# Kernel optimization log

Hardware: AMD Instinct MI355X
Metric: run time of the kernel (lower is better)

The kernel has to match this reference:

```python
import jax, jax.numpy as jnp
import numpy as np

B, L, D, H, S, V, K = 2, 64, 1024, 512, 50000, 40000, 32
SLM_LOGITS_SCALE = 0.1
BN_EPS = 1e-5


def setup_inputs() -> dict:
    key = jax.random.key(0)
    ks = jax.random.split(key, 8)
    return {
        "cached_embeddings": jax.random.normal(ks[0], (B, L, D), dtype=jnp.float32),
        "bn_gamma": jnp.ones((L,), jnp.float32),
        "bn_beta": jnp.zeros((L,), jnp.float32),
        "W1": jax.random.normal(ks[1], (D, H), dtype=jnp.float32) * 0.02,
        "b1": jnp.zeros((H,), jnp.float32),
        "W2": jax.random.normal(ks[2], (H, S), dtype=jnp.float32) * 0.02,
        "b2": jnp.zeros((S,), jnp.float32),
        "W_slm": jax.random.normal(ks[3], (H, V), dtype=jnp.float32) * 0.02,
        "b_slm": jnp.zeros((V,), jnp.float32),
        # fixed degree k=32 with values 1/min(deg,k) = 1/32 (full-degree rows)
        "sl_weights": jnp.full((S, K), 1.0 / K, jnp.float32),
        "sl_idx": jax.random.randint(ks[4], (S, K), 0, V, dtype=jnp.int32),
    }


def reference(cached_embeddings, bn_gamma, bn_beta, W1, b1, W2, b2,
              W_slm, b_slm, sl_weights, sl_idx):
    x = cached_embeddings  # [B, L, D]
    # BatchNorm1d(win_size): channels are sequence positions; stats over (B, D)
    mean = jnp.mean(x, axis=(0, 2), keepdims=True)
    var = jnp.var(x, axis=(0, 2), keepdims=True)
    xn = (x - mean) * jax.lax.rsqrt(var + BN_EPS)
    x = xn * bn_gamma[None, :, None] + bn_beta[None, :, None]
    # DenseEncoder: hidden + sense logits
    h = jax.nn.relu(jnp.einsum('bld,dh->blh', x, W1) + b1)  # [B, L, H]
    y = jnp.einsum('blh,hs->bls', h, W2) + b2                # [B, L, S]
    # SLM head: lemma logits
    v = jnp.einsum('blh,hv->blv', h, W_slm) + b_slm          # [B, L, V]
    # sparse sense->lemma matmul == weighted bounded-degree gather-sum
    g = v[..., sl_idx]                                       # [B, L, S, K]
    slm_logits = jnp.einsum('blsk,sk->bls', g, sl_weights)   # [B, L, S]
    return y + slm_logits * SLM_LOGITS_SCALE
```

## Files before the change

kernel.cpp:

```cpp
#include <hip/hip_runtime.h>

#define LL 64
#define DD 1024
#define HH 512
#define SS 50000
#define VV 40000
#define KD 32
#define MM 128

typedef __bf16 bf16_t;
typedef __bf16 bf16x8 __attribute__((ext_vector_type(8)));
typedef __bf16 bf16x4 __attribute__((ext_vector_type(4)));
typedef __bf16 bf16x2 __attribute__((ext_vector_type(2)));
typedef float f32x4 __attribute__((ext_vector_type(4)));

__device__ __forceinline__ void async_ld16(const void* g, void* l) {
    __builtin_amdgcn_global_load_lds(
        (const __attribute__((address_space(1))) void*)g,
        (__attribute__((address_space(3))) void*)l, 16, 0, 0);
}

#define WAITV(N) asm volatile("s_waitcnt vmcnt(" #N ")" ::: "memory")

__device__ __forceinline__ void bn_body(int l, const float* __restrict__ x,
        const float* __restrict__ gamma, const float* __restrict__ beta,
        bf16_t* __restrict__ xn) {
    int t = threadIdx.x;
    int b = t >> 7;
    int d0 = (t & 127) << 3;
    const float* xp = x + (size_t)(b * LL + l) * DD + d0;
    float4 v0 = *(const float4*)xp;
    float4 v1 = *(const float4*)(xp + 4);
    float s  = v0.x + v0.y + v0.z + v0.w + v1.x + v1.y + v1.z + v1.w;
    float ss = v0.x*v0.x + v0.y*v0.y + v0.z*v0.z + v0.w*v0.w
             + v1.x*v1.x + v1.y*v1.y + v1.z*v1.z + v1.w*v1.w;
    #pragma unroll
    for (int off = 32; off > 0; off >>= 1) {
        s  += __shfl_xor(s, off);
        ss += __shfl_xor(ss, off);
    }
    __shared__ float red[8];
    int wv = t >> 6, ln = t & 63;
    if (ln == 0) { red[wv] = s; red[4 + wv] = ss; }
    __syncthreads();
    float tot  = red[0] + red[1] + red[2] + red[3];
    float tots = red[4] + red[5] + red[6] + red[7];
    float mean = tot * (1.0f / 2048.0f);
    float var  = tots * (1.0f / 2048.0f) - mean * mean;
    float rstd = rsqrtf(var + 1e-5f);
    float g   = gamma[l] * rstd;
    float ofs = beta[l] - mean * g;
    bf16x8 o;
    o[0] = (bf16_t)(v0.x * g + ofs);
    o[1] = (bf16_t)(v0.y * g + ofs);
    o[2] = (bf16_t)(v0.z * g + ofs);
    o[3] = (bf16_t)(v0.w * g + ofs);
    o[4] = (bf16_t)(v1.x * g + ofs);
    o[5] = (bf16_t)(v1.y * g + ofs);
    o[6] = (bf16_t)(v1.z * g + ofs);
    o[7] = (bf16_t)(v1.w * g + ofs);
    *(bf16x8*)(xn + (size_t)(b * LL + l) * DD + d0) = o;
}

__device__ __forceinline__ void conv_body(const float* __restrict__ src,
        bf16_t* __restrict__ dst, int p, int s) {
    int t = threadIdx.x;
    #pragma unroll
    for (int half = 0; half < 2; ++half) {
        int cid = t + half * 256;
        int cc = cid & 15, qq = (cid >> 4) & 3, wvv = (cid >> 6) & 3, ns = cid >> 8;
        int col = p * 128 + ns * 64 + wvv * 16 + cc;
        int k0 = s * 32 + qq * 8;
        bf16x8 o;
        #pragma unroll
        for (int i = 0; i < 8; ++i)
            o[i] = (bf16_t)src[(size_t)(k0 + i) * HH + col];
        *(bf16x8*)(dst + ((size_t)(p * 32 + s) * 512 + cid) * 8) = o;
    }
}

__global__ __launch_bounds__(256) void k_prep(const float* __restrict__ x,
        const float* __restrict__ gamma, const float* __restrict__ beta,
        bf16_t* __restrict__ xn, const float* __restrict__ W1,
        bf16_t* __restrict__ W1p) {
    int bid = blockIdx.x;
    if (bid < 64) { bn_body(bid, x, gamma, beta, xn); return; }
    int u = bid - 64;
    conv_body(W1, W1p, u >> 5, u & 31);
}

__global__ __launch_bounds__(64) void k_gemm1(const bf16_t* __restrict__ xn,
        const bf16_t* __restrict__ W1p, const float* __restrict__ b1,
        bf16_t* __restrict__ h) {
    int lane = threadIdx.x & 63;
    int c = lane & 15, q = lane >> 4;
    int tile = blockIdx.x;
    int tm = tile >> 5, tn = tile & 31;
    int p = tn >> 3, ns = (tn >> 2) & 1, wvv = tn & 3;
    const bf16_t* wp = W1p + ((size_t)(p * 32) * 512 + ns * 256 + wvv * 64 + q * 16 + c) * 8;
    const bf16_t* ap = xn + (size_t)(tm * 16 + c) * DD + q * 8;
    f32x4 acc = {};
    #pragma unroll 4
    for (int st = 0; st < 32; ++st) {
        bf16x8 bfr = *(const bf16x8*)(wp + (size_t)st * 4096);
        bf16x8 afr = *(const bf16x8*)(ap + st * 32);
        acc = __builtin_amdgcn_mfma_f32_16x16x32_bf16(afr, bfr, acc, 0, 0, 0);
    }
    int col = tn * 16 + c;
    float bias = b1[col];
    #pragma unroll
    for (int r = 0; r < 4; ++r) {
        int m = tm * 16 + q * 4 + r;
        float v = acc[r] + bias;
        h[(size_t)m * HH + col] = (bf16_t)(v > 0.f ? v : 0.f);
    }
}

__device__ __forceinline__ void gemm_wide(const bf16_t* __restrict__ A,
        const float* __restrict__ Wnb , int NC, int nb,
        char* smem, f32x4 (&acc)[8][2]) {
    int t = threadIdx.x;
    int lane = t & 63, wv = t >> 6;
    int c = lane & 15, q = lane >> 4;
    const float* gw[4];
    #pragma unroll
    for (int r = 0; r < 4; ++r) {
        int i = t + r * 512;
        int coff = (i & 63) * 4;
        if (nb + coff + 4 > NC) coff = NC - nb - 4;
        gw[r] = Wnb + (size_t)(i >> 6) * NC + coff;
    }
    const bf16_t* gh = A + (size_t)(((t >> 6) << 4) + (t & 15)) * HH + ((t >> 4) & 3) * 8;

    #define STG(buf, st) do { \
        char* sb = smem + (buf) * 40960; \
        async_ld16(gw[0] + (size_t)(st) * 32 * NC, sb + (size_t)t * 16); \
        async_ld16(gw[1] + (size_t)(st) * 32 * NC, sb + (size_t)(t + 512) * 16); \
        async_ld16(gw[2] + (size_t)(st) * 32 * NC, sb + (size_t)(t + 1024) * 16); \
        async_ld16(gw[3] + (size_t)(st) * 32 * NC, sb + (size_t)(t + 1536) * 16); \
        async_ld16(gh + (st) * 32, sb + 32768 + (size_t)t * 16); } while (0)

    STG(0, 0); STG(1, 1);

    auto comp = [&](int cur) {
        char* sb = smem + cur * 40960;
        const float*  wl = (const float*)sb;
        const bf16_t* al = (const bf16_t*)(sb + 32768);
        bf16x8 bf0, bf1;
        #pragma unroll
        for (int j = 0; j < 8; ++j) {
            bf0[j] = (bf16_t)wl[(q * 8 + j) * 256 + wv * 32 + c];
            bf1[j] = (bf16_t)wl[(q * 8 + j) * 256 + wv * 32 + 16 + c];
        }
        #pragma unroll
        for (int ms = 0; ms < 8; ++ms) {
            bf16x8 afr = *(const bf16x8*)(al + (size_t)(ms * 64 + lane) * 8);
            acc[ms][0] = __builtin_amdgcn_mfma_f32_16x16x32_bf16(afr, bf0, acc[ms][0], 0, 0, 0);
            acc[ms][1] = __builtin_amdgcn_mfma_f32_16x16x32_bf16(afr, bf1, acc[ms][1], 0, 0, 0);
        }
    };

    #pragma unroll 1
    for (int st = 0; st < 14; ++st) {
        WAITV(5);
        __builtin_amdgcn_s_barrier();
        comp(st & 1);
        __builtin_amdgcn_s_barrier();
        STG(st & 1, st + 2);
    }
    WAITV(5); __builtin_amdgcn_s_barrier(); comp(0);
    WAITV(0); __builtin_amdgcn_s_barrier(); comp(1);
    #undef STG
}

__global__ __launch_bounds__(512) void k_gemm_v(const bf16_t* __restrict__ h,
        const float* __restrict__ Wslm, const float* __restrict__ bslm,
        bf16_t* __restrict__ vT) {
    __shared__ __align__(16) char smem[2 * 40960];
    int nb = blockIdx.x * 256;
    f32x4 acc[8][2] = {};
    gemm_wide(h, Wslm + nb, VV, nb, smem, acc);
    int t = threadIdx.x, lane = t & 63, wv = t >> 6;
    int c = lane & 15, q = lane >> 4;
    #pragma unroll
    for (int ns = 0; ns < 2; ++ns) {
        int col = nb + wv * 32 + ns * 16 + c;
        if (col < VV) {
            float bias = bslm[col];
            #pragma unroll
            for (int ms = 0; ms < 8; ++ms) {
                bf16x4 o;
                #pragma unroll
                for (int rr = 0; rr < 4; ++rr) o[rr] = (bf16_t)(acc[ms][ns][rr] + bias);
                *(bf16x4*)(vT + (size_t)col * MM + ms * 16 + q * 4) = o;
            }
        }
    }
}

__global__ __launch_bounds__(256) void k_gather(const bf16_t* __restrict__ vT,
        const float* __restrict__ slw, const int* __restrict__ slidx,
        bf16_t* __restrict__ slm) {
    int t = threadIdx.x;
    int wv = t >> 6, lane = t & 63;
    int s = blockIdx.x * 4 + wv;
    int idv = slidx[(size_t)s * KD + (lane & 31)];
    float wgt = slw[(size_t)s * KD + (lane & 31)];
    unsigned int u[KD];
    #pragma unroll
    for (int k = 0; k < KD; ++k) {
        int id = __shfl(idv, k);
        u[k] = *(const unsigned int*)(vT + (size_t)id * MM + lane * 2);
    }
    float a0 = 0.f, a1 = 0.f;
    #pragma unroll
    for (int k = 0; k < KD; ++k) {
        float w = __shfl(wgt, k);
        a0 += w * __uint_as_float(u[k] << 16);
        a1 += w * __uint_as_float(u[k] & 0xffff0000u);
    }
    bf16x2 o;
    o[0] = (bf16_t)a0;
    o[1] = (bf16_t)a1;
    *(bf16x2*)(slm + (size_t)s * MM + lane * 2) = o;
}

__global__ __launch_bounds__(512) void k_gemm_y(const bf16_t* __restrict__ h,
        const float* __restrict__ W2, const float* __restrict__ b2,
        const bf16_t* __restrict__ slm, float* __restrict__ out) {
    __shared__ __align__(16) char smem[2 * 40960];
    int nb = blockIdx.x * 256;
    f32x4 acc[8][2] = {};
    gemm_wide(h, W2 + nb, SS, nb, smem, acc);
    int t = threadIdx.x, lane = t & 63, wv = t >> 6;
    int c = lane & 15, q = lane >> 4;
    #pragma unroll
    for (int ns = 0; ns < 2; ++ns) {
        int col = nb + wv * 32 + ns * 16 + c;
        if (col < SS) {
            float bias = b2[col];
            #pragma unroll
            for (int ms = 0; ms < 8; ++ms) {
                bf16x4 sv = *(const bf16x4*)(slm + (size_t)col * MM + ms * 16 + q * 4);
                #pragma unroll
                for (int rr = 0; rr < 4; ++rr) {
                    int m = ms * 16 + q * 4 + rr;
                    out[(size_t)m * SS + col] = acc[ms][ns][rr] + bias + 0.1f * (float)sv[rr];
                }
            }
        }
    }
}

extern "C" void kernel_launch(void* const* d_in, const int* in_sizes, int n_in,
                              void* d_out, int out_size, void* d_ws, size_t ws_size,
                              hipStream_t stream) {
    const float* x     = (const float*)d_in[0];
    const float* gamma = (const float*)d_in[1];
    const float* beta  = (const float*)d_in[2];
    const float* W1    = (const float*)d_in[3];
    const float* b1    = (const float*)d_in[4];
    const float* W2    = (const float*)d_in[5];
    const float* b2    = (const float*)d_in[6];
    const float* Wslm  = (const float*)d_in[7];
    const float* bslm  = (const float*)d_in[8];
    const float* slw   = (const float*)d_in[9];
    const int*   slidx = (const int*)d_in[10];
    float* out = (float*)d_out;

    char* ws = (char*)d_ws;
    bf16_t* xn  = (bf16_t*)ws;
    bf16_t* h   = (bf16_t*)(ws + 262144);
    bf16_t* vT  = (bf16_t*)(ws + 393216);
    bf16_t* slm = (bf16_t*)(ws + 10633216);
    bf16_t* W1p = (bf16_t*)(ws + 23433216);

    k_prep  <<<192,   256, 0, stream>>>(x, gamma, beta, xn, W1, W1p);
    k_gemm1 <<<256,   64,  0, stream>>>(xn, W1p, b1, h);
    k_gemm_v<<<157,   512, 0, stream>>>(h, Wslm, bslm, vT);
    k_gather<<<12500, 256, 0, stream>>>(vT, slw, slidx, slm);
    k_gemm_y<<<196,   512, 0, stream>>>(h, W2, b2, slm, out);
}
```

Baseline: 292.8 us.

## Widen gather loads to 16 bytes and stage output tile through LDS for coalesced stores

The gather kernel now handles four senses per wavefront. Each 16-lane group loads 16-byte chunks of a vT row, instead of each lane loading 4 bytes, which cuts the number of memory transactions per gathered row. The y GEMM epilogue adds the slm term into the accumulators, then writes each 16-row slab through a shared-memory tile so that every thread stores contiguous float4 vectors with the bias added. The old epilogue scattered scalar stores across the 50000-wide output. The trade-offs are more registers held in the gather (16 uint4 values), extra LDS traffic, and barriers inside the store loop.

```diff
diff --git a/kernel.cpp b/kernel.cpp
--- a/kernel.cpp
+++ b/kernel.cpp
@@ -203,26 +203,54 @@
         bf16_t* __restrict__ slm) {
     int t = threadIdx.x;
     int wv = t >> 6, lane = t & 63;
-    int s = blockIdx.x * 4 + wv;
-    int idv = slidx[(size_t)s * KD + (lane & 31)];
-    float wgt = slw[(size_t)s * KD + (lane & 31)];
-    unsigned int u[KD];
-    #pragma unroll
-    for (int k = 0; k < KD; ++k) {
-        int id = __shfl(idv, k);
-        u[k] = *(const unsigned int*)(vT + (size_t)id * MM + lane * 2);
-    }
-    float a0 = 0.f, a1 = 0.f;
-    #pragma unroll
-    for (int k = 0; k < KD; ++k) {
-        float w = __shfl(wgt, k);
-        a0 += w * __uint_as_float(u[k] << 16);
-        a1 += w * __uint_as_float(u[k] & 0xffff0000u);
-    }
-    bf16x2 o;
-    o[0] = (bf16_t)a0;
-    o[1] = (bf16_t)a1;
-    *(bf16x2*)(slm + (size_t)s * MM + lane * 2) = o;
+    int grp = lane >> 4, li = lane & 15;
+    int s = blockIdx.x * 16 + wv * 4 + grp;
+    int   id0 = slidx[(size_t)s * KD + li];
+    int   id1 = slidx[(size_t)s * KD + 16 + li];
+    float wg0 = slw[(size_t)s * KD + li];
+    float wg1 = slw[(size_t)s * KD + 16 + li];
+    float a[8] = {};
+    uint4 u[16];
+    #pragma unroll
+    for (int k = 0; k < 16; ++k) {
+        int id = __shfl(id0, grp * 16 + k);
+        u[k] = *(const uint4*)(vT + (size_t)id * MM + li * 8);
+    }
+    #pragma unroll
+    for (int k = 0; k < 16; ++k) {
+        float w = __shfl(wg0, grp * 16 + k);
+        unsigned uu0 = u[k].x, uu1 = u[k].y, uu2 = u[k].z, uu3 = u[k].w;
+        a[0] += w * __uint_as_float(uu0 << 16);
+        a[1] += w * __uint_as_float(uu0 & 0xffff0000u);
+        a[2] += w * __uint_as_float(uu1 << 16);
+        a[3] += w * __uint_as_float(uu1 & 0xffff0000u);
+        a[4] += w * __uint_as_float(uu2 << 16);
+        a[5] += w * __uint_as_float(uu2 & 0xffff0000u);
+        a[6] += w * __uint_as_float(uu3 << 16);
+        a[7] += w * __uint_as_float(uu3 & 0xffff0000u);
+    }
+    #pragma unroll
+    for (int k = 0; k < 16; ++k) {
+        int id = __shfl(id1, grp * 16 + k);
+        u[k] = *(const uint4*)(vT + (size_t)id * MM + li * 8);
+    }
+    #pragma unroll
+    for (int k = 0; k < 16; ++k) {
+        float w = __shfl(wg1, grp * 16 + k);
+        unsigned uu0 = u[k].x, uu1 = u[k].y, uu2 = u[k].z, uu3 = u[k].w;
+        a[0] += w * __uint_as_float(uu0 << 16);
+        a[1] += w * __uint_as_float(uu0 & 0xffff0000u);
+        a[2] += w * __uint_as_float(uu1 << 16);
+        a[3] += w * __uint_as_float(uu1 & 0xffff0000u);
+        a[4] += w * __uint_as_float(uu2 << 16);
+        a[5] += w * __uint_as_float(uu2 & 0xffff0000u);
+        a[6] += w * __uint_as_float(uu3 << 16);
+        a[7] += w * __uint_as_float(uu3 & 0xffff0000u);
+    }
+    bf16x8 o;
+    #pragma unroll
+    for (int j = 0; j < 8; ++j) o[j] = (bf16_t)a[j];
+    *(bf16x8*)(slm + (size_t)s * MM + li * 8) = o;
 }
 
 __global__ __launch_bounds__(512) void k_gemm_y(const bf16_t* __restrict__ h,
@@ -238,17 +266,48 @@
     for (int ns = 0; ns < 2; ++ns) {
         int col = nb + wv * 32 + ns * 16 + c;
         if (col < SS) {
-            float bias = b2[col];
             #pragma unroll
             for (int ms = 0; ms < 8; ++ms) {
                 bf16x4 sv = *(const bf16x4*)(slm + (size_t)col * MM + ms * 16 + q * 4);
                 #pragma unroll
-                for (int rr = 0; rr < 4; ++rr) {
-                    int m = ms * 16 + q * 4 + rr;
-                    out[(size_t)m * SS + col] = acc[ms][ns][rr] + bias + 0.1f * (float)sv[rr];
-                }
+                for (int rr = 0; rr < 4; ++rr)
+                    acc[ms][ns][rr] += 0.1f * (float)sv[rr];
             }
         }
+    }
+    float* tile = (float*)smem;
+    int r = t >> 5, col0 = (t & 31) * 8;
+    bool fullblk = (nb + 256 <= SS);
+    float4 bb0 = {}, bb1 = {};
+    if (fullblk) {
+        bb0 = *(const float4*)(b2 + nb + col0);
+        bb1 = *(const float4*)(b2 + nb + col0 + 4);
+    }
+    #pragma unroll 1
+    for (int ms = 0; ms < 8; ++ms) {
+        #pragma unroll
+        for (int ns = 0; ns < 2; ++ns)
+            #pragma unroll
+            for (int rr = 0; rr < 4; ++rr)
+                tile[(q * 4 + rr) * 260 + wv * 32 + ns * 16 + c] = acc[ms][ns][rr];
+        __syncthreads();
+        int m = ms * 16 + r;
+        if (fullblk) {
+            float4 v0 = *(const float4*)&tile[r * 260 + col0];
+            float4 v1 = *(const float4*)&tile[r * 260 + col0 + 4];
+            v0.x += bb0.x; v0.y += bb0.y; v0.z += bb0.z; v0.w += bb0.w;
+            v1.x += bb1.x; v1.y += bb1.y; v1.z += bb1.z; v1.w += bb1.w;
+            *(float4*)(out + (size_t)m * SS + nb + col0) = v0;
+            *(float4*)(out + (size_t)m * SS + nb + col0 + 4) = v1;
+        } else {
+            #pragma unroll
+            for (int j = 0; j < 8; ++j) {
+                int col = nb + col0 + j;
+                if (col < SS)
+                    out[(size_t)m * SS + col] = tile[r * 260 + col0 + j] + b2[col];
+            }
+        }
+        __syncthreads();
     }
 }
 
@@ -275,9 +334,9 @@
     bf16_t* slm = (bf16_t*)(ws + 10633216);
     bf16_t* W1p = (bf16_t*)(ws + 23433216);
 
-    k_prep  <<<192,   256, 0, stream>>>(x, gamma, beta, xn, W1, W1p);
-    k_gemm1 <<<256,   64,  0, stream>>>(xn, W1p, b1, h);
-    k_gemm_v<<<157,   512, 0, stream>>>(h, Wslm, bslm, vT);
-    k_gather<<<12500, 256, 0, stream>>>(vT, slw, slidx, slm);
-    k_gemm_y<<<196,   512, 0, stream>>>(h, W2, b2, slm, out);
-}
+    k_prep  <<<192,  256, 0, stream>>>(x, gamma, beta, xn, W1, W1p);
+    k_gemm1 <<<256,  64,  0, stream>>>(xn, W1p, b1, h);
+    k_gemm_v<<<157,  512, 0, stream>>>(h, Wslm, bslm, vT);
+    k_gather<<<3125, 256, 0, stream>>>(vT, slw, slidx, slm);
+    k_gemm_y<<<196,  512, 0, stream>>>(h, W2, b2, slm, out);
+}
```

After: 322.0 us. 10.0% more time.
